# Performance work log

Measured on AMD Instinct MI355X. Metric: run time of the kernel, lower is better.

## Reference

```python
import jax, jax.numpy as jnp
import numpy as np
import math

B, L, D, H = 2, 2048, 1024, 16
HD = D // H

def setup_inputs() -> dict:
    key = jax.random.key(0)
    ks = jax.random.split(key, 8)
    s = 1.0 / math.sqrt(D)
    # causal additive mask: 0 on/below diagonal, -inf above
    causal = jnp.where(jnp.tril(jnp.ones((L, L), dtype=bool)), 0.0, -jnp.inf)
    causal = causal[None, None].astype(jnp.float32)  # [1,1,L,L]
    return {
        "Q": jax.random.normal(ks[0], (B, L, D), jnp.float32),
        "K": jax.random.normal(ks[1], (B, L, D), jnp.float32),
        "V": jax.random.normal(ks[2], (B, L, D), jnp.float32),
        "attn_mask": causal,
        "padding_mask": jnp.zeros((B, L), dtype=bool),
        "wq": jax.random.normal(ks[3], (D, D), jnp.float32) * s,
        "wk": jax.random.normal(ks[4], (D, D), jnp.float32) * s,
        "wv": jax.random.normal(ks[5], (D, D), jnp.float32) * s,
        "wout": jax.random.normal(ks[6], (D, D), jnp.float32) * s,
    }

def reference(Q, K, V, attn_mask, padding_mask, wq, wk, wv, wout):
    b, l, _ = Q.shape
    # projections (torch Linear: x @ W.T); weights sampled as [out,in]-like square
    def proj(x, w):
        return (x @ w.T).reshape(b, l, H, HD).transpose(0, 2, 1, 3)  # [B,H,L,hd]
    q = proj(Q, wq)
    k = proj(K, wk)
    v = proj(V, wv)
    scores = jnp.einsum("bhqd,bhkd->bhqk", q, k) / math.sqrt(HD)
    scores = scores + attn_mask
    scores = jnp.where(padding_mask[:, None, None, :], -jnp.inf, scores)
    weights = jax.nn.softmax(scores, axis=-1)
    ctx = jnp.einsum("bhqk,bhkd->bhqd", weights, v)
    ctx = ctx.transpose(0, 2, 1, 3).reshape(b, l, D)
    return ctx @ wout.T
```

## Files before the change

kernel.cpp:

```cpp
#include <hip/hip_runtime.h>
#include <stdint.h>
#include <stddef.h>

typedef __bf16 bf16_t;
typedef bf16_t bf16x4 __attribute__((ext_vector_type(4)));
typedef bf16_t bf16x8 __attribute__((ext_vector_type(8)));
typedef float f32x4 __attribute__((ext_vector_type(4)));

#define MFMA_BF16(A_, B_, C_) __builtin_amdgcn_mfma_f32_16x16x32_bf16(A_, B_, C_, 0, 0, 0)

static constexpr int Lseq = 2048;
static constexpr int Dmod = 1024;
static constexpr int Hn   = 16;
static constexpr int HDim = 64;
static constexpr size_t M1 = 1u << 20;

__device__ __forceinline__ int swz(int row, int chunk) {
  return row * 64 + ((chunk ^ (row & 7)) << 3);
}

__device__ __forceinline__ void async_ld16(const bf16_t* g, bf16_t* l) {
  __builtin_amdgcn_global_load_lds(
      (const __attribute__((address_space(1))) void*)g,
      (__attribute__((address_space(3))) void*)l, 16, 0, 0);
}

__global__ __launch_bounds__(256) void cvt_kernel(
    const float* __restrict__ Q, const float* __restrict__ K,
    const float* __restrict__ V, const float* __restrict__ wq,
    const float* __restrict__ wk, const float* __restrict__ wv,
    const float* __restrict__ wout, bf16_t* __restrict__ wsb)
{
  const int s = blockIdx.z;
  const float* __restrict__ src;
  if      (s < 4)   src = Q    + (size_t)s * M1;
  else if (s < 8)   src = K    + (size_t)(s - 4) * M1;
  else if (s < 12)  src = V    + (size_t)(s - 8) * M1;
  else if (s == 12) src = wq;
  else if (s == 13) src = wk;
  else if (s == 14) src = wv;
  else              src = wout;
  bf16_t* __restrict__ dst = wsb + (size_t)s * M1;
  const float scale = (s == 12) ? 0.18033688f : 1.0f;

  const int idx = blockIdx.x * 256 + threadIdx.x;
  float4 a = ((const float4*)src)[idx * 2];
  float4 b = ((const float4*)src)[idx * 2 + 1];
  bf16x8 o;
  o[0] = (bf16_t)(a.x * scale); o[1] = (bf16_t)(a.y * scale);
  o[2] = (bf16_t)(a.z * scale); o[3] = (bf16_t)(a.w * scale);
  o[4] = (bf16_t)(b.x * scale); o[5] = (bf16_t)(b.y * scale);
  o[6] = (bf16_t)(b.z * scale); o[7] = (bf16_t)(b.w * scale);
  ((bf16x8*)dst)[idx] = o;
}

__global__ __launch_bounds__(256) void proj_kernel(
    const bf16_t* __restrict__ Qbf, const bf16_t* __restrict__ Kbf,
    const bf16_t* __restrict__ Vbf, const bf16_t* __restrict__ wqb,
    const bf16_t* __restrict__ wkb, const bf16_t* __restrict__ wvb,
    bf16_t* __restrict__ qo, bf16_t* __restrict__ ko, bf16_t* __restrict__ vo)
{
  const int z = blockIdx.z;
  const bf16_t* __restrict__ A  = (z == 0) ? Qbf : (z == 1) ? Kbf : Vbf;
  const bf16_t* __restrict__ Bw = (z == 0) ? wqb : (z == 1) ? wkb : wvb;
  bf16_t* __restrict__ dst      = (z == 0) ? qo  : (z == 1) ? ko  : vo;

  __shared__ __align__(16) bf16_t As[128 * 64];
  __shared__ __align__(16) bf16_t Bs[64 * 64];

  const int tid  = threadIdx.x;
  const int wave = tid >> 6;
  const int lane = tid & 63;
  const int quad = lane >> 4;
  const int l16  = lane & 15;
  const int wm   = (wave & 1) * 64;
  const int wn   = (wave >> 1) * 32;
  const int m0   = blockIdx.x * 128;
  const int n0   = blockIdx.y * 64;

  const int srow8  = lane >> 3;
  const int schunk = (lane & 7) ^ srow8;

  f32x4 acc[4][2];
#pragma unroll
  for (int i = 0; i < 4; ++i)
#pragma unroll
    for (int j = 0; j < 2; ++j)
#pragma unroll
      for (int e = 0; e < 4; ++e) acc[i][j][e] = 0.0f;

  for (int kt = 0; kt < 16; ++kt) {
    const int k0 = kt * 64;
    __syncthreads();
#pragma unroll
    for (int i = 0; i < 4; ++i) {
      const int rb = wave * 32 + i * 8;
      async_ld16(&A[(size_t)(m0 + rb + srow8) * Dmod + k0 + schunk * 8], &As[rb * 64]);
    }
#pragma unroll
    for (int i = 0; i < 2; ++i) {
      const int rb = wave * 16 + i * 8;
      async_ld16(&Bw[(size_t)(n0 + rb + srow8) * Dmod + k0 + schunk * 8], &Bs[rb * 64]);
    }
    __syncthreads();

    bf16x8 af[4][2], bfr[2][2];
#pragma unroll
    for (int mt = 0; mt < 4; ++mt) {
      const int row = wm + mt * 16 + l16;
      af[mt][0] = *(const bf16x8*)&As[swz(row, quad)];
      af[mt][1] = *(const bf16x8*)&As[swz(row, quad + 4)];
    }
#pragma unroll
    for (int nt = 0; nt < 2; ++nt) {
      const int row = wn + nt * 16 + l16;
      bfr[nt][0] = *(const bf16x8*)&Bs[swz(row, quad)];
      bfr[nt][1] = *(const bf16x8*)&Bs[swz(row, quad + 4)];
    }
#pragma unroll
    for (int mt = 0; mt < 4; ++mt)
#pragma unroll
      for (int nt = 0; nt < 2; ++nt) {
        acc[mt][nt] = MFMA_BF16(af[mt][0], bfr[nt][0], acc[mt][nt]);
        acc[mt][nt] = MFMA_BF16(af[mt][1], bfr[nt][1], acc[mt][nt]);
      }
  }

#pragma unroll
  for (int mt = 0; mt < 4; ++mt) {
    const int grb = m0 + wm + mt * 16 + quad * 4;
    const int bb  = grb >> 11;
    const int lb  = grb & 2047;
#pragma unroll
    for (int nt = 0; nt < 2; ++nt) {
      const int gc = n0 + wn + nt * 16 + l16;
      const int h  = gc >> 6;
      const int hd = gc & 63;
      if (z == 2) {
        bf16x4 pk;
#pragma unroll
        for (int r = 0; r < 4; ++r) pk[r] = (bf16_t)acc[mt][nt][r];
        *(bf16x4*)&dst[(((size_t)(bb * Hn + h) * HDim + hd) << 11) + lb] = pk;
      } else {
#pragma unroll
        for (int r = 0; r < 4; ++r)
          dst[(((size_t)(bb * Hn + h) * Lseq + lb + r) << 6) + hd] = (bf16_t)acc[mt][nt][r];
      }
    }
  }
}

__global__ __launch_bounds__(256) void attn_kernel(
    const bf16_t* __restrict__ q, const bf16_t* __restrict__ k,
    const bf16_t* __restrict__ v, bf16_t* __restrict__ ctx)
{
  const int bh = blockIdx.x;
  const int px = blockIdx.y;
  const int bb = bh >> 4;
  const int h  = bh & 15;

  const int tid  = threadIdx.x;
  const int wave = tid >> 6;
  const int lane = tid & 63;
  const int quad = lane >> 4;
  const int l16  = lane & 15;

  __shared__ __align__(16) bf16_t Ks[2][64 * 64];
  __shared__ __align__(16) bf16_t Vs[2][64 * 64];
  __shared__ __align__(16) bf16_t Ps[4][16][72];

  const bf16_t* __restrict__ qb = q + (size_t)bh * (Lseq * HDim);
  const bf16_t* __restrict__ kb = k + (size_t)bh * (Lseq * HDim);
  const bf16_t* __restrict__ vb = v + (size_t)bh * (HDim * Lseq);

  const int srow8  = lane >> 3;
  const int schunk = (lane & 7) ^ srow8;

  bf16x8 ones;
#pragma unroll
  for (int i = 0; i < 8; ++i) ones[i] = (bf16_t)1.0f;

  for (int half = 0; half < 2; ++half) {
    const int qt = half ? (31 - px) : px;
    const int q0 = qt * 64;
    const int qrow = q0 + wave * 16 + l16;

    bf16x8 qf0 = *(const bf16x8*)&qb[(size_t)qrow * HDim + quad * 8];
    bf16x8 qf1 = *(const bf16x8*)&qb[(size_t)qrow * HDim + 32 + quad * 8];

    f32x4 o[4];
    f32x4 lacc;
#pragma unroll
    for (int e = 0; e < 4; ++e) lacc[e] = 0.0f;
#pragma unroll
    for (int nt = 0; nt < 4; ++nt)
#pragma unroll
      for (int e = 0; e < 4; ++e) o[nt][e] = 0.0f;

    __syncthreads();
#pragma unroll
    for (int i = 0; i < 2; ++i) {
      const int rb = wave * 16 + i * 8;
      const int r  = rb + srow8;
      async_ld16(&kb[(size_t)r * HDim + schunk * 8], &Ks[0][rb * 64]);
      async_ld16(&vb[(size_t)r * Lseq + schunk * 8], &Vs[0][rb * 64]);
    }

    for (int jt = 0; jt <= qt; ++jt) {
      const int cur = jt & 1;
      __syncthreads();

      if (jt < qt) {
        const int j1 = (jt + 1) * 64;
#pragma unroll
        for (int i = 0; i < 2; ++i) {
          const int rb = wave * 16 + i * 8;
          const int r  = rb + srow8;
          async_ld16(&kb[(size_t)(j1 + r) * HDim + schunk * 8], &Ks[cur ^ 1][rb * 64]);
          async_ld16(&vb[(size_t)r * Lseq + j1 + schunk * 8], &Vs[cur ^ 1][rb * 64]);
        }
      }

      f32x4 s[4];
#pragma unroll
      for (int nt = 0; nt < 4; ++nt) {
#pragma unroll
        for (int e = 0; e < 4; ++e) s[nt][e] = 0.0f;
        const int krow = nt * 16 + l16;
        bf16x8 kf0 = *(const bf16x8*)&Ks[cur][swz(krow, quad)];
        bf16x8 kf1 = *(const bf16x8*)&Ks[cur][swz(krow, quad + 4)];
        s[nt] = MFMA_BF16(kf0, qf0, s[nt]);
        s[nt] = MFMA_BF16(kf1, qf1, s[nt]);
      }

      const bool diag = (jt == qt);
#pragma unroll
      for (int nt = 0; nt < 4; ++nt) {
        bf16x4 pk;
#pragma unroll
        for (int r = 0; r < 4; ++r) {
          float val = s[nt][r];
          if (diag && (nt * 16 + quad * 4 + r > wave * 16 + l16)) val = -1e30f;
          pk[r] = (bf16_t)__builtin_amdgcn_exp2f(val);
        }
        *(bf16x4*)&Ps[wave][l16][nt * 16 + quad * 4] = pk;
      }

      bf16x8 pf0 = *(const bf16x8*)&Ps[wave][l16][quad * 8];
      bf16x8 pf1 = *(const bf16x8*)&Ps[wave][l16][32 + quad * 8];

      lacc = MFMA_BF16(pf0, ones, lacc);
      lacc = MFMA_BF16(pf1, ones, lacc);

#pragma unroll
      for (int nt = 0; nt < 4; ++nt) {
        const int vrow = nt * 16 + l16;
        bf16x8 vf0 = *(const bf16x8*)&Vs[cur][swz(vrow, quad)];
        bf16x8 vf1 = *(const bf16x8*)&Vs[cur][swz(vrow, quad + 4)];
        o[nt] = MFMA_BF16(pf0, vf0, o[nt]);
        o[nt] = MFMA_BF16(pf1, vf1, o[nt]);
      }
    }

    float inv[4];
#pragma unroll
    for (int r = 0; r < 4; ++r) inv[r] = 1.0f / lacc[r];
#pragma unroll
    for (int nt = 0; nt < 4; ++nt)
#pragma unroll
      for (int r = 0; r < 4; ++r) {
        const int gq = q0 + wave * 16 + quad * 4 + r;
        ctx[(size_t)(bb * Lseq + gq) * Dmod + h * HDim + nt * 16 + l16] =
            (bf16_t)(o[nt][r] * inv[r]);
      }
  }
}

__global__ __launch_bounds__(256) void out_kernel(
    const bf16_t* __restrict__ Actx, const bf16_t* __restrict__ Bwout,
    float* __restrict__ out)
{
  __shared__ __align__(16) bf16_t As[128 * 64];
  __shared__ __align__(16) bf16_t Bs[64 * 64];

  const int tid  = threadIdx.x;
  const int wave = tid >> 6;
  const int lane = tid & 63;
  const int quad = lane >> 4;
  const int l16  = lane & 15;
  const int wm   = (wave & 1) * 64;
  const int wn   = (wave >> 1) * 32;
  const int m0   = blockIdx.x * 128;
  const int n0   = blockIdx.y * 64;

  const int srow8  = lane >> 3;
  const int schunk = (lane & 7) ^ srow8;

  f32x4 acc[4][2];
#pragma unroll
  for (int i = 0; i < 4; ++i)
#pragma unroll
    for (int j = 0; j < 2; ++j)
#pragma unroll
      for (int e = 0; e < 4; ++e) acc[i][j][e] = 0.0f;

  for (int kt = 0; kt < 16; ++kt) {
    const int k0 = kt * 64;
    __syncthreads();
#pragma unroll
    for (int i = 0; i < 4; ++i) {
      const int rb = wave * 32 + i * 8;
      async_ld16(&Actx[(size_t)(m0 + rb + srow8) * Dmod + k0 + schunk * 8], &As[rb * 64]);
    }
#pragma unroll
    for (int i = 0; i < 2; ++i) {
      const int rb = wave * 16 + i * 8;
      async_ld16(&Bwout[(size_t)(n0 + rb + srow8) * Dmod + k0 + schunk * 8], &Bs[rb * 64]);
    }
    __syncthreads();

    bf16x8 af[4][2], bfr[2][2];
#pragma unroll
    for (int mt = 0; mt < 4; ++mt) {
      const int row = wm + mt * 16 + l16;
      af[mt][0] = *(const bf16x8*)&As[swz(row, quad)];
      af[mt][1] = *(const bf16x8*)&As[swz(row, quad + 4)];
    }
#pragma unroll
    for (int nt = 0; nt < 2; ++nt) {
      const int row = wn + nt * 16 + l16;
      bfr[nt][0] = *(const bf16x8*)&Bs[swz(row, quad)];
      bfr[nt][1] = *(const bf16x8*)&Bs[swz(row, quad + 4)];
    }
#pragma unroll
    for (int mt = 0; mt < 4; ++mt)
#pragma unroll
      for (int nt = 0; nt < 2; ++nt) {
        acc[mt][nt] = MFMA_BF16(af[mt][0], bfr[nt][0], acc[mt][nt]);
        acc[mt][nt] = MFMA_BF16(af[mt][1], bfr[nt][1], acc[mt][nt]);
      }
  }

#pragma unroll
  for (int mt = 0; mt < 4; ++mt) {
    const int grb = m0 + wm + mt * 16 + quad * 4;
#pragma unroll
    for (int nt = 0; nt < 2; ++nt) {
      const int gc = n0 + wn + nt * 16 + l16;
#pragma unroll
      for (int r = 0; r < 4; ++r)
        out[(size_t)(grb + r) * Dmod + gc] = acc[mt][nt][r];
    }
  }
}

extern "C" void kernel_launch(void* const* d_in, const int* in_sizes, int n_in,
                              void* d_out, int out_size, void* d_ws, size_t ws_size,
                              hipStream_t stream) {
  (void)in_sizes; (void)n_in; (void)out_size; (void)ws_size;
  const float* Q    = (const float*)d_in[0];
  const float* K    = (const float*)d_in[1];
  const float* V    = (const float*)d_in[2];
  const float* wq   = (const float*)d_in[5];
  const float* wk   = (const float*)d_in[6];
  const float* wv   = (const float*)d_in[7];
  const float* wout = (const float*)d_in[8];
  float* out = (float*)d_out;

  bf16_t* wsb = (bf16_t*)d_ws;
  bf16_t* Qbf   = wsb;
  bf16_t* Kbf   = wsb + 4 * M1;
  bf16_t* Vbf   = wsb + 8 * M1;
  bf16_t* wqb   = wsb + 12 * M1;
  bf16_t* wkb   = wsb + 13 * M1;
  bf16_t* wvb   = wsb + 14 * M1;
  bf16_t* woutb = wsb + 15 * M1;
  bf16_t* qp    = wsb + 16 * M1;
  bf16_t* kp    = wsb + 20 * M1;
  bf16_t* vp    = wsb + 24 * M1;
  bf16_t* cws   = wsb;

  cvt_kernel<<<dim3(512, 1, 16), 256, 0, stream>>>(Q, K, V, wq, wk, wv, wout, wsb);
  proj_kernel<<<dim3(32, 16, 3), 256, 0, stream>>>(Qbf, Kbf, Vbf, wqb, wkb, wvb, qp, kp, vp);
  attn_kernel<<<dim3(32, 16), 256, 0, stream>>>(qp, kp, vp, cws);
  out_kernel<<<dim3(32, 16), 256, 0, stream>>>(cws, woutb, out);
}
```

Measured before the change: 213.7 us.

## Launch one block per query tile and drop K/V double buffering in attention

The attention kernel used to pair query tiles (px and 31-px) inside one block. It now launches one block per query tile, longest tiles first, on a 32x32 grid, which doubles the block count. K/V shared memory goes from double-buffered to single-buffered, with a sync before and after each synchronous tile load, so load latency is no longer overlapped with compute. The goal is more parallelism and lower LDS use for higher occupancy. The cost is exposed load latency and possible load imbalance across blocks.

```diff
diff --git a/kernel.cpp b/kernel.cpp
--- a/kernel.cpp
+++ b/kernel.cpp
@@ -155,9 +155,10 @@
     const bf16_t* __restrict__ v, bf16_t* __restrict__ ctx)
 {
   const int bh = blockIdx.x;
-  const int px = blockIdx.y;
+  const int qt = 31 - blockIdx.y;
   const int bb = bh >> 4;
   const int h  = bh & 15;
+  const int q0 = qt * 64;
 
   const int tid  = threadIdx.x;
   const int wave = tid >> 6;
@@ -165,8 +166,8 @@
   const int quad = lane >> 4;
   const int l16  = lane & 15;
 
-  __shared__ __align__(16) bf16_t Ks[2][64 * 64];
-  __shared__ __align__(16) bf16_t Vs[2][64 * 64];
+  __shared__ __align__(16) bf16_t Ks[64 * 64];
+  __shared__ __align__(16) bf16_t Vs[64 * 64];
   __shared__ __align__(16) bf16_t Ps[4][16][72];
 
   const bf16_t* __restrict__ qb = q + (size_t)bh * (Lseq * HDim);
@@ -180,100 +181,83 @@
 #pragma unroll
   for (int i = 0; i < 8; ++i) ones[i] = (bf16_t)1.0f;
 
-  for (int half = 0; half < 2; ++half) {
-    const int qt = half ? (31 - px) : px;
-    const int q0 = qt * 64;
-    const int qrow = q0 + wave * 16 + l16;
-
-    bf16x8 qf0 = *(const bf16x8*)&qb[(size_t)qrow * HDim + quad * 8];
-    bf16x8 qf1 = *(const bf16x8*)&qb[(size_t)qrow * HDim + 32 + quad * 8];
-
-    f32x4 o[4];
-    f32x4 lacc;
-#pragma unroll
-    for (int e = 0; e < 4; ++e) lacc[e] = 0.0f;
-#pragma unroll
-    for (int nt = 0; nt < 4; ++nt)
-#pragma unroll
-      for (int e = 0; e < 4; ++e) o[nt][e] = 0.0f;
-
+  const int qrow = q0 + wave * 16 + l16;
+  bf16x8 qf0 = *(const bf16x8*)&qb[(size_t)qrow * HDim + quad * 8];
+  bf16x8 qf1 = *(const bf16x8*)&qb[(size_t)qrow * HDim + 32 + quad * 8];
+
+  f32x4 o[4];
+  f32x4 lacc;
+#pragma unroll
+  for (int e = 0; e < 4; ++e) lacc[e] = 0.0f;
+#pragma unroll
+  for (int nt = 0; nt < 4; ++nt)
+#pragma unroll
+    for (int e = 0; e < 4; ++e) o[nt][e] = 0.0f;
+
+  for (int jt = 0; jt <= qt; ++jt) {
+    const int j0 = jt * 64;
     __syncthreads();
 #pragma unroll
     for (int i = 0; i < 2; ++i) {
       const int rb = wave * 16 + i * 8;
       const int r  = rb + srow8;
-      async_ld16(&kb[(size_t)r * HDim + schunk * 8], &Ks[0][rb * 64]);
-      async_ld16(&vb[(size_t)r * Lseq + schunk * 8], &Vs[0][rb * 64]);
-    }
-
-    for (int jt = 0; jt <= qt; ++jt) {
-      const int cur = jt & 1;
-      __syncthreads();
-
-      if (jt < qt) {
-        const int j1 = (jt + 1) * 64;
-#pragma unroll
-        for (int i = 0; i < 2; ++i) {
-          const int rb = wave * 16 + i * 8;
-          const int r  = rb + srow8;
-          async_ld16(&kb[(size_t)(j1 + r) * HDim + schunk * 8], &Ks[cur ^ 1][rb * 64]);
-          async_ld16(&vb[(size_t)r * Lseq + j1 + schunk * 8], &Vs[cur ^ 1][rb * 64]);
-        }
+      async_ld16(&kb[(size_t)(j0 + r) * HDim + schunk * 8], &Ks[rb * 64]);
+      async_ld16(&vb[(size_t)r * Lseq + j0 + schunk * 8], &Vs[rb * 64]);
+    }
+    __syncthreads();
+
+    f32x4 s[4];
+#pragma unroll
+    for (int nt = 0; nt < 4; ++nt) {
+#pragma unroll
+      for (int e = 0; e < 4; ++e) s[nt][e] = 0.0f;
+      const int krow = nt * 16 + l16;
+      bf16x8 kf0 = *(const bf16x8*)&Ks[swz(krow, quad)];
+      bf16x8 kf1 = *(const bf16x8*)&Ks[swz(krow, quad + 4)];
+      s[nt] = MFMA_BF16(kf0, qf0, s[nt]);
+      s[nt] = MFMA_BF16(kf1, qf1, s[nt]);
+    }
+
+    const bool diag = (jt == qt);
+#pragma unroll
+    for (int nt = 0; nt < 4; ++nt) {
+      bf16x4 pk;
+#pragma unroll
+      for (int r = 0; r < 4; ++r) {
+        float val = s[nt][r];
+        if (diag && (nt * 16 + quad * 4 + r > wave * 16 + l16)) val = -1e30f;
+        pk[r] = (bf16_t)__builtin_amdgcn_exp2f(val);
       }
-
-      f32x4 s[4];
-#pragma unroll
-      for (int nt = 0; nt < 4; ++nt) {
-#pragma unroll
-        for (int e = 0; e < 4; ++e) s[nt][e] = 0.0f;
-        const int krow = nt * 16 + l16;
-        bf16x8 kf0 = *(const bf16x8*)&Ks[cur][swz(krow, quad)];
-        bf16x8 kf1 = *(const bf16x8*)&Ks[cur][swz(krow, quad + 4)];
-        s[nt] = MFMA_BF16(kf0, qf0, s[nt]);
-        s[nt] = MFMA_BF16(kf1, qf1, s[nt]);
-      }
-
-      const bool diag = (jt == qt);
-#pragma unroll
-      for (int nt = 0; nt < 4; ++nt) {
-        bf16x4 pk;
-#pragma unroll
-        for (int r = 0; r < 4; ++r) {
-          float val = s[nt][r];
-          if (diag && (nt * 16 + quad * 4 + r > wave * 16 + l16)) val = -1e30f;
-          pk[r] = (bf16_t)__builtin_amdgcn_exp2f(val);
-        }
-        *(bf16x4*)&Ps[wave][l16][nt * 16 + quad * 4] = pk;
-      }
-
-      bf16x8 pf0 = *(const bf16x8*)&Ps[wave][l16][quad * 8];
-      bf16x8 pf1 = *(const bf16x8*)&Ps[wave][l16][32 + quad * 8];
-
-      lacc = MFMA_BF16(pf0, ones, lacc);
-      lacc = MFMA_BF16(pf1, ones, lacc);
-
-#pragma unroll
-      for (int nt = 0; nt < 4; ++nt) {
-        const int vrow = nt * 16 + l16;
-        bf16x8 vf0 = *(const bf16x8*)&Vs[cur][swz(vrow, quad)];
-        bf16x8 vf1 = *(const bf16x8*)&Vs[cur][swz(vrow, quad + 4)];
-        o[nt] = MFMA_BF16(pf0, vf0, o[nt]);
-        o[nt] = MFMA_BF16(pf1, vf1, o[nt]);
-      }
-    }
-
-    float inv[4];
-#pragma unroll
-    for (int r = 0; r < 4; ++r) inv[r] = 1.0f / lacc[r];
-#pragma unroll
-    for (int nt = 0; nt < 4; ++nt)
-#pragma unroll
-      for (int r = 0; r < 4; ++r) {
-        const int gq = q0 + wave * 16 + quad * 4 + r;
-        ctx[(size_t)(bb * Lseq + gq) * Dmod + h * HDim + nt * 16 + l16] =
-            (bf16_t)(o[nt][r] * inv[r]);
-      }
-  }
+      *(bf16x4*)&Ps[wave][l16][nt * 16 + quad * 4] = pk;
+    }
+
+    bf16x8 pf0 = *(const bf16x8*)&Ps[wave][l16][quad * 8];
+    bf16x8 pf1 = *(const bf16x8*)&Ps[wave][l16][32 + quad * 8];
+
+    lacc = MFMA_BF16(pf0, ones, lacc);
+    lacc = MFMA_BF16(pf1, ones, lacc);
+
+#pragma unroll
+    for (int nt = 0; nt < 4; ++nt) {
+      const int vrow = nt * 16 + l16;
+      bf16x8 vf0 = *(const bf16x8*)&Vs[swz(vrow, quad)];
+      bf16x8 vf1 = *(const bf16x8*)&Vs[swz(vrow, quad + 4)];
+      o[nt] = MFMA_BF16(pf0, vf0, o[nt]);
+      o[nt] = MFMA_BF16(pf1, vf1, o[nt]);
+    }
+  }
+
+  float inv[4];
+#pragma unroll
+  for (int r = 0; r < 4; ++r) inv[r] = 1.0f / lacc[r];
+#pragma unroll
+  for (int nt = 0; nt < 4; ++nt)
+#pragma unroll
+    for (int r = 0; r < 4; ++r) {
+      const int gq = q0 + wave * 16 + quad * 4 + r;
+      ctx[(size_t)(bb * Lseq + gq) * Dmod + h * HDim + nt * 16 + l16] =
+          (bf16_t)(o[nt][r] * inv[r]);
+    }
 }
 
 __global__ __launch_bounds__(256) void out_kernel(
@@ -382,6 +366,6 @@
 
   cvt_kernel<<<dim3(512, 1, 16), 256, 0, stream>>>(Q, K, V, wq, wk, wv, wout, wsb);
   proj_kernel<<<dim3(32, 16, 3), 256, 0, stream>>>(Qbf, Kbf, Vbf, wqb, wkb, wvb, qp, kp, vp);
-  attn_kernel<<<dim3(32, 16), 256, 0, stream>>>(qp, kp, vp, cws);
+  attn_kernel<<<dim3(32, 32), 256, 0, stream>>>(qp, kp, vp, cws);
   out_kernel<<<dim3(32, 16), 256, 0, stream>>>(cws, woutb, out);
 }
```

Result: no change. 212.6 us (-0.5%).
